# Kernel optimization log

Hardware: AMD Instinct MI355X
Metric: run time of the kernel (lower is better)

The kernel has to match this reference:

```python
import jax, jax.numpy as jnp
import numpy as np
from jax.scipy.special import logsumexp

N = 512   # hidden states (obs_number)
M = 256   # emission symbols == sequence length (raw_number)
B = 128   # batch


def setup_inputs() -> dict:
    key = jax.random.key(0)
    k1, k2, k3, k4 = jax.random.split(key, 4)
    return {
        "obs": jax.random.randint(k1, (B, M), 0, M),
        "unnormalized_state_priors": jax.random.normal(k2, (N,), dtype=jnp.float32),
        "unnormalized_transition_matrix": jax.random.normal(k3, (N, N), dtype=jnp.float32),
        "unnormalized_emission_matrix": jax.random.normal(k4, (N, M), dtype=jnp.float32),
    }


def reference(obs, unnormalized_state_priors, unnormalized_transition_matrix,
              unnormalized_emission_matrix):
    # Normalized matrices are computed ONCE (the torch code redundantly
    # recomputes them every timestep; the math is identical).
    log_priors = jax.nn.log_softmax(unnormalized_state_priors)                 # [N]
    log_T = jax.nn.log_softmax(unnormalized_transition_matrix, axis=0)         # [N,N], T[i,k]=P(i|k)
    log_E = jax.nn.log_softmax(unnormalized_emission_matrix, axis=1)           # [N,M]

    # Emission log-probs per timestep: em[b,t,i] = log_E[i, obs[b,t]] -> [B,M,N]
    em = jnp.moveaxis(log_E[:, obs], 0, -1)

    alpha0 = em[:, 0, :] + log_priors                                          # [B,N]

    def step(a_prev, e_t):
        # log-domain matmul: a[b,i] = logsumexp_k( log_T[i,k] + a_prev[b,k] )
        a = e_t + logsumexp(log_T[None, :, :] + a_prev[:, None, :], axis=-1)   # [B,N]
        return a, logsumexp(a, axis=-1)                                        # carry, per-t log-sum

    em_tm = jnp.swapaxes(em, 0, 1)                                             # time-major [M,B,N]
    _, ls_rest = jax.lax.scan(step, alpha0, em_tm[1:])                         # [M-1,B]

    ls0 = logsumexp(alpha0, axis=-1)                                           # [B]
    log_sums = jnp.concatenate([ls0[:, None], ls_rest.T], axis=1)              # [B,M]
    return log_sums
```

## Files before the change

### kernel.cpp

```cpp
#include <hip/hip_runtime.h>
#include <hip/hip_bf16.h>
#include <math.h>

#define NN 512
#define MM 256
#define BB 128

typedef float        f32x4 __attribute__((ext_vector_type(4)));
typedef unsigned int u32;
typedef u32          u32x2 __attribute__((ext_vector_type(2)));
typedef unsigned long long u64;
typedef int          i32x8 __attribute__((ext_vector_type(8)));

#define LOG16F 2.772588722239781f
#define SCL1   0x7F

__device__ __forceinline__ float wave_max(float v) {
#pragma unroll
    for (int o = 32; o > 0; o >>= 1) v = fmaxf(v, __shfl_xor(v, o));
    return v;
}
__device__ __forceinline__ float wave_sum(float v) {
#pragma unroll
    for (int o = 32; o > 0; o >>= 1) v += __shfl_xor(v, o);
    return v;
}


__global__ void k_col_lse(const float* __restrict__ T, float* __restrict__ c) {
    int k = blockIdx.x, j = threadIdx.x;
    float m = -INFINITY, s = 0.f;
#pragma unroll
    for (int q = 0; q < 8; ++q) {
        float x = T[(q * 64 + j) * NN + k];
        if (x > m) { s = s * __expf(m - x) + 1.f; m = x; }
        else       { s += __expf(x - m); }
    }
    float mw = wave_max(m);
    float sw = wave_sum(s * __expf(m - mw));
    if (j == 0) c[k] = mw + __logf(sw);
}

__global__ void k_rowM(const float* __restrict__ T, const float* __restrict__ c,
                       float* __restrict__ M) {
    int i = blockIdx.x, j = threadIdx.x;
    float mx = -INFINITY;
#pragma unroll
    for (int d = 0; d < 8; ++d) {
        int k = j * 8 + d;
        mx = fmaxf(mx, T[i * NN + k] - c[k]);
    }
    mx = wave_max(mx);
    if (j == 0) M[i] = mx - __logf(64.f);
}

__global__ void k_prep(const float* __restrict__ T, const float* __restrict__ c,
                       const float* __restrict__ M, const float* __restrict__ pr,
                       const float* __restrict__ E,
                       float* __restrict__ lp2, u32* __restrict__ PA,
                       float* __restrict__ EX) {
    int blk = blockIdx.x, l = threadIdx.x;
    if (blk < 512) {
        float mm = -INFINITY;
#pragma unroll
        for (int q = 0; q < 8; ++q) mm = fmaxf(mm, M[q * 64 + l]);
        float CMv = wave_max(mm);
        int i = blk;
        float v[4];
        float mx = -INFINITY;
#pragma unroll
        for (int d = 0; d < 4; ++d) {
            v[d] = E[i * MM + l * 4 + d];
            mx = fmaxf(mx, v[d]);
        }
        mx = wave_max(mx);
        float s = 0.f;
#pragma unroll
        for (int d = 0; d < 4; ++d) s += __expf(v[d] - mx);
        s = wave_sum(s);
        float lse = mx + __logf(s);
        float add = M[i] - CMv - LOG16F - lse;
#pragma unroll
        for (int d = 0; d < 4; ++d)
            EX[(size_t)(l * 4 + d) * NN + i] = __expf(v[d] + add);
    } else if (blk < 640) {
        int bb = blk - 512;
        int tile = bb >> 2, kc = bb & 3;
        int row = tile * 16 + (l & 15);
        int kb  = kc * 128 + (l >> 4) * 32;
        float Mi = M[row];
        i32x8 dd;
#pragma unroll
        for (int q = 0; q < 8; ++q) {
            float p0 = __expf(T[row * NN + kb + 4*q + 0] - c[kb + 4*q + 0] - Mi);
            float p1 = __expf(T[row * NN + kb + 4*q + 1] - c[kb + 4*q + 1] - Mi);
            float p2 = __expf(T[row * NN + kb + 4*q + 2] - c[kb + 4*q + 2] - Mi);
            float p3 = __expf(T[row * NN + kb + 4*q + 3] - c[kb + 4*q + 3] - Mi);
            int d = 0;
            d = __builtin_amdgcn_cvt_pk_fp8_f32(p0, p1, d, false);
            d = __builtin_amdgcn_cvt_pk_fp8_f32(p2, p3, d, true);
            dd[q] = d;
        }
        *(i32x8*)(PA + ((size_t)bb * 64 + l) * 8) = dd;
    } else {
        float mm = -INFINITY;
#pragma unroll
        for (int q = 0; q < 8; ++q) mm = fmaxf(mm, M[q * 64 + l]);
        float CMv = wave_max(mm);
        float x[8];
        float mx = -INFINITY;
#pragma unroll
        for (int q = 0; q < 8; ++q) {
            x[q] = pr[q * 64 + l];
            mx = fmaxf(mx, x[q]);
        }
        mx = wave_max(mx);
        float s = 0.f;
#pragma unroll
        for (int q = 0; q < 8; ++q) s += __expf(x[q] - mx);
        s = wave_sum(s);
        float lse = mx + __logf(s);
#pragma unroll
        for (int q = 0; q < 8; ++q) {
            int i = q * 64 + l;
            lp2[i] = __expf(x[q] - lse - M[i] + CMv + LOG16F);
        }
    }
}

__global__ __launch_bounds__(512, 2) void k_scan(
        const int* __restrict__ obs, const float* __restrict__ lp2,
        const float* __restrict__ Mrow, const u32* __restrict__ PAu,
        const float* __restrict__ EX, float* __restrict__ out) {
    int b = blockIdx.x, tid = threadIdx.x;
    int w = tid >> 6, l = tid & 63;
    int h32 = (l >> 4) * 32;
    int r4 = (l >> 4) * 4;
    __shared__ unsigned char us8[NN] __attribute__((aligned(64)));
    __shared__ float rB[8] __attribute__((aligned(16)));
    __shared__ int obs_s[MM];
    if (tid < MM) obs_s[tid] = obs[b * MM + tid];

    float mm = -INFINITY;
#pragma unroll
    for (int q = 0; q < 8; ++q) mm = fmaxf(mm, Mrow[q * 64 + l]);
    float C_M = wave_max(mm);

    i32x8 pa[16];
#pragma unroll
    for (int ti = 0; ti < 4; ++ti)
#pragma unroll
        for (int kc = 0; kc < 4; ++kc)
            pa[ti * 4 + kc] = *(const i32x8*)(PAu
                + ((size_t)(((w * 4 + ti) * 4 + kc) * 64) + l) * 8);
#pragma unroll
    for (int q = 0; q < 16; ++q) asm volatile("" : "+a"(pa[q]));

    int ubase[4];
#pragma unroll
    for (int ti = 0; ti < 4; ++ti) ubase[ti] = (w * 4 + ti) * 16 + r4;
    __syncthreads();

    int o0 = obs_s[0];
    f32x4 e4[4];
    float loc = 0.f;
#pragma unroll
    for (int ti = 0; ti < 4; ++ti) {
        f32x4 ex  = *(const f32x4*)(EX  + (size_t)o0 * NN + (w * 4 + ti) * 16 + r4);
        f32x4 lpv = *(const f32x4*)(lp2 + (w * 4 + ti) * 16 + r4);
#pragma unroll
        for (int r = 0; r < 4; ++r) {
            float e = ex[r] * lpv[r];
            e4[ti][r] = e; loc += e;
        }
    }
    loc += __shfl_xor(loc, 16);
    loc += __shfl_xor(loc, 32);
    if (l == 0) rB[w] = loc;
    __syncthreads();
    f32x4 sv0 = *(const f32x4*)rB;
    f32x4 sv1 = *(const f32x4*)(rB + 4);
    float S = (sv0[0] + sv0[1]) + (sv0[2] + sv0[3])
            + (sv1[0] + sv1[1]) + (sv1[2] + sv1[3]);
    S = fmaxf(S, 1e-35f);
    float sc = __builtin_amdgcn_rcpf(S) * 16.f;
    if ((l & 15) == 0) {
#pragma unroll
        for (int ti = 0; ti < 4; ++ti) {
            int d = 0;
            d = __builtin_amdgcn_cvt_pk_fp8_f32(e4[ti][0] * sc, e4[ti][1] * sc, d, false);
            d = __builtin_amdgcn_cvt_pk_fp8_f32(e4[ti][2] * sc, e4[ti][3] * sc, d, true);
            *(u32*)&us8[ubase[ti]] = (u32)d;
        }
    }
    __syncthreads();
    float lS = __logf(S);
    if (tid == 0) out[(size_t)b * MM + 0] = lS;
    float K = C_M + lS;

    f32x4 exn[4];
    {
        int on = obs_s[1];
#pragma unroll
        for (int ti = 0; ti < 4; ++ti)
            exn[ti] = *(const f32x4*)(EX + (size_t)on * NN + (w * 4 + ti) * 16 + r4);
    }

#pragma unroll 1
    for (int t = 1; t < MM; ++t) {
        const unsigned char* ub = us8;
        f32x4 a0 = {0.f,0.f,0.f,0.f}, a1 = {0.f,0.f,0.f,0.f};
        f32x4 a2 = {0.f,0.f,0.f,0.f}, a3 = {0.f,0.f,0.f,0.f};
        f32x4 b0 = {0.f,0.f,0.f,0.f}, b1 = {0.f,0.f,0.f,0.f};
        f32x4 b2 = {0.f,0.f,0.f,0.f}, b3 = {0.f,0.f,0.f,0.f};
        __builtin_amdgcn_s_setprio(1);
#pragma unroll
        for (int kc = 0; kc < 2; ++kc) {
            i32x8 bbA = *(const i32x8*)(ub + kc * 128 + h32);
            i32x8 bbB = *(const i32x8*)(ub + (kc + 2) * 128 + h32);
            a0 = __builtin_amdgcn_mfma_scale_f32_16x16x128_f8f6f4(
                     pa[0 * 4 + kc], bbA, a0, 0, 0, 0, SCL1, 0, SCL1);
            a1 = __builtin_amdgcn_mfma_scale_f32_16x16x128_f8f6f4(
                     pa[1 * 4 + kc], bbA, a1, 0, 0, 0, SCL1, 0, SCL1);
            a2 = __builtin_amdgcn_mfma_scale_f32_16x16x128_f8f6f4(
                     pa[2 * 4 + kc], bbA, a2, 0, 0, 0, SCL1, 0, SCL1);
            a3 = __builtin_amdgcn_mfma_scale_f32_16x16x128_f8f6f4(
                     pa[3 * 4 + kc], bbA, a3, 0, 0, 0, SCL1, 0, SCL1);
            b0 = __builtin_amdgcn_mfma_scale_f32_16x16x128_f8f6f4(
                     pa[0 * 4 + kc + 2], bbB, b0, 0, 0, 0, SCL1, 0, SCL1);
            b1 = __builtin_amdgcn_mfma_scale_f32_16x16x128_f8f6f4(
                     pa[1 * 4 + kc + 2], bbB, b1, 0, 0, 0, SCL1, 0, SCL1);
            b2 = __builtin_amdgcn_mfma_scale_f32_16x16x128_f8f6f4(
                     pa[2 * 4 + kc + 2], bbB, b2, 0, 0, 0, SCL1, 0, SCL1);
            b3 = __builtin_amdgcn_mfma_scale_f32_16x16x128_f8f6f4(
                     pa[3 * 4 + kc + 2], bbB, b3, 0, 0, 0, SCL1, 0, SCL1);
        }
        __builtin_amdgcn_s_setprio(0);
        f32x4 sacc[4] = { a0 + b0, a1 + b1, a2 + b2, a3 + b3 };

        loc = 0.f;
#pragma unroll
        for (int ti = 0; ti < 4; ++ti)
#pragma unroll
            for (int r = 0; r < 4; ++r) {
                float e = exn[ti][r] * sacc[ti][r];
                e4[ti][r] = e; loc += e;
            }

        int on = obs_s[(t + 1 < MM) ? t + 1 : t];
#pragma unroll
        for (int ti = 0; ti < 4; ++ti)
            exn[ti] = *(const f32x4*)(EX + (size_t)on * NN + (w * 4 + ti) * 16 + r4);

        loc += __shfl_xor(loc, 16);
        loc += __shfl_xor(loc, 32);
        if (l == 0) rB[w] = loc;
        __syncthreads();
        sv0 = *(const f32x4*)rB;
        sv1 = *(const f32x4*)(rB + 4);
        S = (sv0[0] + sv0[1]) + (sv0[2] + sv0[3])
          + (sv1[0] + sv1[1]) + (sv1[2] + sv1[3]);
        S = fmaxf(S, 1e-35f);
        sc = __builtin_amdgcn_rcpf(S) * 16.f;
        if ((l & 15) == 0) {
#pragma unroll
            for (int ti = 0; ti < 4; ++ti) {
                int d = 0;
                d = __builtin_amdgcn_cvt_pk_fp8_f32(e4[ti][0] * sc, e4[ti][1] * sc, d, false);
                d = __builtin_amdgcn_cvt_pk_fp8_f32(e4[ti][2] * sc, e4[ti][3] * sc, d, true);
                *(u32*)&us8[ubase[ti]] = (u32)d;
            }
        }
        __syncthreads();
        float lSn = __logf(S);
        if (tid == 0) out[(size_t)b * MM + t] = K + lSn;
        K += C_M + lSn;
    }
}

extern "C" void kernel_launch(void* const* d_in, const int* in_sizes, int n_in,
                              void* d_out, int out_size, void* d_ws, size_t ws_size,
                              hipStream_t stream) {
    const int*   obs = (const int*)d_in[0];
    const float* pri = (const float*)d_in[1];
    const float* T   = (const float*)d_in[2];
    const float* E   = (const float*)d_in[3];
    float* out = (float*)d_out;
    char* ws = (char*)d_ws;

    float* c   = (float*)(ws + 0);
    float* lp2 = (float*)(ws + 2048);
    float* M   = (float*)(ws + 4096);
    u32*   PA  = (u32*)(ws + 8192);
    float* EX  = (float*)(ws + 8192 + 256 * 1024);

    k_col_lse<<<512, 64, 0, stream>>>(T, c);
    k_rowM   <<<512, 64, 0, stream>>>(T, c, M);
    k_prep   <<<641, 64, 0, stream>>>(T, c, M, pri, E, lp2, PA, EX);
    k_scan   <<<BB, 512, 0, stream>>>(obs, lp2, M, PA, EX, out);
}
```

Baseline: 327.1 us.

## Use predicted power-of-two fp8 scale to drop one barrier per scan step

The scan no longer quantizes the next alpha vector to fp8 using the exact block sum from the same step, which needed a reduction and barrier before quantizing. It now uses a power-of-two scale predicted from a smoothed max exponent of earlier steps, and double-buffers the fp8 state and reduction buffers so each steady-state step needs one __syncthreads instead of two. The log-normalizer bookkeeping is changed to account for the power-of-two scale. The trade-off is precision risk: a stale exponent estimate with clamping at 448 could saturate or underflow fp8 values.

```diff
diff --git a/kernel.cpp b/kernel.cpp
--- a/kernel.cpp
+++ b/kernel.cpp
@@ -13,6 +13,7 @@
 typedef int          i32x8 __attribute__((ext_vector_type(8)));
 
 #define LOG16F 2.772588722239781f
+#define LN2F   0.6931471805599453f
 #define SCL1   0x7F
 
 __device__ __forceinline__ float wave_max(float v) {
@@ -24,6 +25,9 @@
 #pragma unroll
     for (int o = 32; o > 0; o >>= 1) v += __shfl_xor(v, o);
     return v;
+}
+__device__ __forceinline__ int fexp(float x) {
+    return ((__float_as_int(x) >> 23) & 255) - 127;
 }
 
 
@@ -136,8 +140,9 @@
     int w = tid >> 6, l = tid & 63;
     int h32 = (l >> 4) * 32;
     int r4 = (l >> 4) * 4;
-    __shared__ unsigned char us8[NN] __attribute__((aligned(64)));
-    __shared__ float rB[8] __attribute__((aligned(16)));
+    __shared__ unsigned char us8[2][NN] __attribute__((aligned(64)));
+    __shared__ float rB[2][8] __attribute__((aligned(16)));
+    __shared__ int   rEm[2][8] __attribute__((aligned(16)));
     __shared__ int obs_s[MM];
     if (tid < MM) obs_s[tid] = obs[b * MM + tid];
 
@@ -176,10 +181,10 @@
     }
     loc += __shfl_xor(loc, 16);
     loc += __shfl_xor(loc, 32);
-    if (l == 0) rB[w] = loc;
+    if (l == 0) rB[0][w] = loc;
     __syncthreads();
-    f32x4 sv0 = *(const f32x4*)rB;
-    f32x4 sv1 = *(const f32x4*)(rB + 4);
+    f32x4 sv0 = *(const f32x4*)rB[0];
+    f32x4 sv1 = *(const f32x4*)(rB[0] + 4);
     float S = (sv0[0] + sv0[1]) + (sv0[2] + sv0[3])
             + (sv1[0] + sv1[1]) + (sv1[2] + sv1[3]);
     S = fmaxf(S, 1e-35f);
@@ -190,7 +195,7 @@
             int d = 0;
             d = __builtin_amdgcn_cvt_pk_fp8_f32(e4[ti][0] * sc, e4[ti][1] * sc, d, false);
             d = __builtin_amdgcn_cvt_pk_fp8_f32(e4[ti][2] * sc, e4[ti][3] * sc, d, true);
-            *(u32*)&us8[ubase[ti]] = (u32)d;
+            *(u32*)&us8[0][ubase[ti]] = (u32)d;
         }
     }
     __syncthreads();
@@ -206,9 +211,12 @@
             exn[ti] = *(const f32x4*)(EX + (size_t)on * NN + (w * 4 + ti) * 16 + r4);
     }
 
+    int W = 0;
+
 #pragma unroll 1
-    for (int t = 1; t < MM; ++t) {
-        const unsigned char* ub = us8;
+    for (int t = 1; t <= 2; ++t) {
+        int p = t & 1, pr = p ^ 1;
+        const unsigned char* ub = us8[pr];
         f32x4 a0 = {0.f,0.f,0.f,0.f}, a1 = {0.f,0.f,0.f,0.f};
         f32x4 a2 = {0.f,0.f,0.f,0.f}, a3 = {0.f,0.f,0.f,0.f};
         f32x4 b0 = {0.f,0.f,0.f,0.f}, b1 = {0.f,0.f,0.f,0.f};
@@ -218,46 +226,42 @@
         for (int kc = 0; kc < 2; ++kc) {
             i32x8 bbA = *(const i32x8*)(ub + kc * 128 + h32);
             i32x8 bbB = *(const i32x8*)(ub + (kc + 2) * 128 + h32);
-            a0 = __builtin_amdgcn_mfma_scale_f32_16x16x128_f8f6f4(
-                     pa[0 * 4 + kc], bbA, a0, 0, 0, 0, SCL1, 0, SCL1);
-            a1 = __builtin_amdgcn_mfma_scale_f32_16x16x128_f8f6f4(
-                     pa[1 * 4 + kc], bbA, a1, 0, 0, 0, SCL1, 0, SCL1);
-            a2 = __builtin_amdgcn_mfma_scale_f32_16x16x128_f8f6f4(
-                     pa[2 * 4 + kc], bbA, a2, 0, 0, 0, SCL1, 0, SCL1);
-            a3 = __builtin_amdgcn_mfma_scale_f32_16x16x128_f8f6f4(
-                     pa[3 * 4 + kc], bbA, a3, 0, 0, 0, SCL1, 0, SCL1);
-            b0 = __builtin_amdgcn_mfma_scale_f32_16x16x128_f8f6f4(
-                     pa[0 * 4 + kc + 2], bbB, b0, 0, 0, 0, SCL1, 0, SCL1);
-            b1 = __builtin_amdgcn_mfma_scale_f32_16x16x128_f8f6f4(
-                     pa[1 * 4 + kc + 2], bbB, b1, 0, 0, 0, SCL1, 0, SCL1);
-            b2 = __builtin_amdgcn_mfma_scale_f32_16x16x128_f8f6f4(
-                     pa[2 * 4 + kc + 2], bbB, b2, 0, 0, 0, SCL1, 0, SCL1);
-            b3 = __builtin_amdgcn_mfma_scale_f32_16x16x128_f8f6f4(
-                     pa[3 * 4 + kc + 2], bbB, b3, 0, 0, 0, SCL1, 0, SCL1);
+            a0 = __builtin_amdgcn_mfma_scale_f32_16x16x128_f8f6f4(pa[0*4+kc],   bbA, a0, 0,0,0, SCL1, 0, SCL1);
+            a1 = __builtin_amdgcn_mfma_scale_f32_16x16x128_f8f6f4(pa[1*4+kc],   bbA, a1, 0,0,0, SCL1, 0, SCL1);
+            a2 = __builtin_amdgcn_mfma_scale_f32_16x16x128_f8f6f4(pa[2*4+kc],   bbA, a2, 0,0,0, SCL1, 0, SCL1);
+            a3 = __builtin_amdgcn_mfma_scale_f32_16x16x128_f8f6f4(pa[3*4+kc],   bbA, a3, 0,0,0, SCL1, 0, SCL1);
+            b0 = __builtin_amdgcn_mfma_scale_f32_16x16x128_f8f6f4(pa[0*4+kc+2], bbB, b0, 0,0,0, SCL1, 0, SCL1);
+            b1 = __builtin_amdgcn_mfma_scale_f32_16x16x128_f8f6f4(pa[1*4+kc+2], bbB, b1, 0,0,0, SCL1, 0, SCL1);
+            b2 = __builtin_amdgcn_mfma_scale_f32_16x16x128_f8f6f4(pa[2*4+kc+2], bbB, b2, 0,0,0, SCL1, 0, SCL1);
+            b3 = __builtin_amdgcn_mfma_scale_f32_16x16x128_f8f6f4(pa[3*4+kc+2], bbB, b3, 0,0,0, SCL1, 0, SCL1);
         }
         __builtin_amdgcn_s_setprio(0);
         f32x4 sacc[4] = { a0 + b0, a1 + b1, a2 + b2, a3 + b3 };
 
         loc = 0.f;
+        float lmax = 0.f;
 #pragma unroll
         for (int ti = 0; ti < 4; ++ti)
 #pragma unroll
             for (int r = 0; r < 4; ++r) {
                 float e = exn[ti][r] * sacc[ti][r];
                 e4[ti][r] = e; loc += e;
+                lmax = fmaxf(lmax, e);
             }
 
-        int on = obs_s[(t + 1 < MM) ? t + 1 : t];
+        int on = obs_s[t + 1];
 #pragma unroll
         for (int ti = 0; ti < 4; ++ti)
             exn[ti] = *(const f32x4*)(EX + (size_t)on * NN + (w * 4 + ti) * 16 + r4);
 
         loc += __shfl_xor(loc, 16);
         loc += __shfl_xor(loc, 32);
-        if (l == 0) rB[w] = loc;
+        lmax = fmaxf(lmax, __shfl_xor(lmax, 16));
+        lmax = fmaxf(lmax, __shfl_xor(lmax, 32));
+        if (l == 0) { rB[p][w] = loc; rEm[p][w] = fexp(fmaxf(lmax, 1e-35f)); }
         __syncthreads();
-        sv0 = *(const f32x4*)rB;
-        sv1 = *(const f32x4*)(rB + 4);
+        sv0 = *(const f32x4*)rB[p];
+        sv1 = *(const f32x4*)(rB[p] + 4);
         S = (sv0[0] + sv0[1]) + (sv0[2] + sv0[3])
           + (sv1[0] + sv1[1]) + (sv1[2] + sv1[3]);
         S = fmaxf(S, 1e-35f);
@@ -268,13 +272,95 @@
                 int d = 0;
                 d = __builtin_amdgcn_cvt_pk_fp8_f32(e4[ti][0] * sc, e4[ti][1] * sc, d, false);
                 d = __builtin_amdgcn_cvt_pk_fp8_f32(e4[ti][2] * sc, e4[ti][3] * sc, d, true);
-                *(u32*)&us8[ubase[ti]] = (u32)d;
+                *(u32*)&us8[p][ubase[ti]] = (u32)d;
             }
         }
         __syncthreads();
         float lSn = __logf(S);
         if (tid == 0) out[(size_t)b * MM + t] = K + lSn;
         K += C_M + lSn;
+        int x = rEm[p][0];
+#pragma unroll
+        for (int j = 1; j < 8; ++j) x = max(x, rEm[p][j]);
+        W = x;
+    }
+
+#pragma unroll 1
+    for (int t = 3; t < MM; ++t) {
+        int p = t & 1, pr = p ^ 1;
+        const unsigned char* ub = us8[pr];
+        f32x4 a0 = {0.f,0.f,0.f,0.f}, a1 = {0.f,0.f,0.f,0.f};
+        f32x4 a2 = {0.f,0.f,0.f,0.f}, a3 = {0.f,0.f,0.f,0.f};
+        f32x4 b0 = {0.f,0.f,0.f,0.f}, b1 = {0.f,0.f,0.f,0.f};
+        f32x4 b2 = {0.f,0.f,0.f,0.f}, b3 = {0.f,0.f,0.f,0.f};
+        __builtin_amdgcn_s_setprio(1);
+#pragma unroll
+        for (int kc = 0; kc < 2; ++kc) {
+            i32x8 bbA = *(const i32x8*)(ub + kc * 128 + h32);
+            i32x8 bbB = *(const i32x8*)(ub + (kc + 2) * 128 + h32);
+            a0 = __builtin_amdgcn_mfma_scale_f32_16x16x128_f8f6f4(pa[0*4+kc],   bbA, a0, 0,0,0, SCL1, 0, SCL1);
+            a1 = __builtin_amdgcn_mfma_scale_f32_16x16x128_f8f6f4(pa[1*4+kc],   bbA, a1, 0,0,0, SCL1, 0, SCL1);
+            a2 = __builtin_amdgcn_mfma_scale_f32_16x16x128_f8f6f4(pa[2*4+kc],   bbA, a2, 0,0,0, SCL1, 0, SCL1);
+            a3 = __builtin_amdgcn_mfma_scale_f32_16x16x128_f8f6f4(pa[3*4+kc],   bbA, a3, 0,0,0, SCL1, 0, SCL1);
+            b0 = __builtin_amdgcn_mfma_scale_f32_16x16x128_f8f6f4(pa[0*4+kc+2], bbB, b0, 0,0,0, SCL1, 0, SCL1);
+            b1 = __builtin_amdgcn_mfma_scale_f32_16x16x128_f8f6f4(pa[1*4+kc+2], bbB, b1, 0,0,0, SCL1, 0, SCL1);
+            b2 = __builtin_amdgcn_mfma_scale_f32_16x16x128_f8f6f4(pa[2*4+kc+2], bbB, b2, 0,0,0, SCL1, 0, SCL1);
+            b3 = __builtin_amdgcn_mfma_scale_f32_16x16x128_f8f6f4(pa[3*4+kc+2], bbB, b3, 0,0,0, SCL1, 0, SCL1);
+        }
+        __builtin_amdgcn_s_setprio(0);
+        f32x4 sacc[4] = { a0 + b0, a1 + b1, a2 + b2, a3 + b3 };
+
+        loc = 0.f;
+        float lmax = 0.f;
+#pragma unroll
+        for (int ti = 0; ti < 4; ++ti)
+#pragma unroll
+            for (int r = 0; r < 4; ++r) {
+                float e = exn[ti][r] * sacc[ti][r];
+                e4[ti][r] = e; loc += e;
+                lmax = fmaxf(lmax, e);
+            }
+
+        float scf = __int_as_float((133 - W) << 23);
+        if ((l & 15) == 0) {
+#pragma unroll
+            for (int ti = 0; ti < 4; ++ti) {
+                float q0 = fminf(e4[ti][0] * scf, 448.f);
+                float q1 = fminf(e4[ti][1] * scf, 448.f);
+                float q2 = fminf(e4[ti][2] * scf, 448.f);
+                float q3 = fminf(e4[ti][3] * scf, 448.f);
+                int d = 0;
+                d = __builtin_amdgcn_cvt_pk_fp8_f32(q0, q1, d, false);
+                d = __builtin_amdgcn_cvt_pk_fp8_f32(q2, q3, d, true);
+                *(u32*)&us8[p][ubase[ti]] = (u32)d;
+            }
+        }
+
+        int on = obs_s[(t + 1 < MM) ? t + 1 : t];
+#pragma unroll
+        for (int ti = 0; ti < 4; ++ti)
+            exn[ti] = *(const f32x4*)(EX + (size_t)on * NN + (w * 4 + ti) * 16 + r4);
+
+        loc += __shfl_xor(loc, 16);
+        loc += __shfl_xor(loc, 32);
+        lmax = fmaxf(lmax, __shfl_xor(lmax, 16));
+        lmax = fmaxf(lmax, __shfl_xor(lmax, 32));
+        if (l == 0) { rB[p][w] = loc; rEm[p][w] = fexp(fmaxf(lmax, 1e-35f)); }
+        __syncthreads();
+
+        sv0 = *(const f32x4*)rB[p];
+        sv1 = *(const f32x4*)(rB[p] + 4);
+        S = (sv0[0] + sv0[1]) + (sv0[2] + sv0[3])
+          + (sv1[0] + sv1[1]) + (sv1[2] + sv1[3]);
+        S = fmaxf(S, 1e-35f);
+        float lSn = __logf(S);
+        if (tid == 0) out[(size_t)b * MM + t] = K + lSn;
+        K += C_M + LOG16F + (float)(W - 6) * LN2F;
+        int x = rEm[p][0];
+#pragma unroll
+        for (int j = 1; j < 8; ++j) x = max(x, rEm[p][j]);
+        W = W + ((x - W) >> 1);
+        W = min(110, max(-110, W));
     }
 }
 
```

Result: no change. 330.4 us (+1.0%).
